# Optimization experiments

Measured on AMD Instinct MI355X. Metric: run time of the kernel, lower is better.

Reference implementation:

```python
import jax, jax.numpy as jnp
import numpy as np

B, S, D, H = 4, 2048, 1024, 16
HD = D // H  # head_dim = 64

def setup_inputs() -> dict:
    key = jax.random.key(0)
    ks = jax.random.split(key, 5)
    scale = 1.0 / np.sqrt(D)
    return {
        "x": jax.random.normal(ks[0], (B, S, D), dtype=jnp.float32),
        "Wqkv": jax.random.normal(ks[1], (D, 3 * D), dtype=jnp.float32) * scale,
        "bqkv": jax.random.normal(ks[2], (3 * D,), dtype=jnp.float32) * 0.01,
        "Wo": jax.random.normal(ks[3], (D, D), dtype=jnp.float32) * scale,
        "bo": jax.random.normal(ks[4], (D,), dtype=jnp.float32) * 0.01,
    }

def reference(x, Wqkv, bqkv, Wo, bo):
    b, s, d = x.shape
    # fused QKV projection: [B,S,3D]
    qkv = jnp.einsum("bsd,de->bse", x, Wqkv) + bqkv
    # [B,S,H,3*HD] -> [B,H,S,3*HD], then chunk into q,k,v per head
    qkv = qkv.reshape(b, s, H, 3 * HD).transpose(0, 2, 1, 3)
    q, k, v = jnp.split(qkv, 3, axis=-1)  # each [B,H,S,HD]
    inv_sqrt_dk = jnp.asarray(1.0 / np.sqrt(HD), dtype=x.dtype)
    scores = jnp.einsum("bhqd,bhkd->bhqk", q, k) * inv_sqrt_dk
    attn = jax.nn.softmax(scores, axis=-1)
    values = jnp.einsum("bhqk,bhkd->bhqd", attn, v)  # [B,H,S,HD]
    # NOTE: source reshapes [B,H,S,HD] -> [B,S,H*HD] WITHOUT permuting back
    # (a quirk of the original code); replicated faithfully.
    values = values.reshape(b, s, d)
    out = jnp.einsum("bsd,de->bse", values, Wo) + bo
    return out
```

## Files before the change

kernel.cpp:

```cpp
#include <hip/hip_runtime.h>
#include <hip/hip_bf16.h>
#include <cstdint>

static constexpr int Bq  = 4;
static constexpr int Sq  = 2048;
static constexpr int Dq  = 1024;
static constexpr int Hq  = 16;
static constexpr int HDq = 64;
static constexpr int ROWS = Bq * Sq;
static constexpr int QKV_N = 3 * Dq;

typedef __bf16 bf16x8 __attribute__((ext_vector_type(8)));
typedef __bf16 bf16x4 __attribute__((ext_vector_type(4)));
typedef __bf16 bf16x2 __attribute__((ext_vector_type(2)));
typedef float  floatx4 __attribute__((ext_vector_type(4)));
typedef float  floatx16 __attribute__((ext_vector_type(16)));
typedef unsigned int uintx4 __attribute__((ext_vector_type(4)));

#define MFMA16(a, b, c) __builtin_amdgcn_mfma_f32_16x16x32_bf16((a), (b), (c), 0, 0, 0)
#define MFMA32(a, b, c) __builtin_amdgcn_mfma_f32_32x32x16_bf16((a), (b), (c), 0, 0, 0)

#define QSCALE 0.18033688011112042f

__device__ __forceinline__ void async16(const void* g, void* l) {
    __builtin_amdgcn_global_load_lds(
        (const __attribute__((address_space(1))) uint32_t*)g,
        (__attribute__((address_space(3))) uint32_t*)l, 16, 0, 0);
}

__global__ __launch_bounds__(256) void prep_kernel(const float4* __restrict__ x4,
                                                   bf16x4* __restrict__ xb4,
                                                   const float* __restrict__ Wqkv,
                                                   __bf16* __restrict__ WqkvT,
                                                   const float* __restrict__ Wo,
                                                   __bf16* __restrict__ WoT) {
    __shared__ float t[32][33];
    const int bx = blockIdx.x;
    if (bx < 8192) {
        int i = bx * 256 + threadIdx.x;
        float4 v = x4[i];
        bf16x4 o;
        o[0] = (__bf16)v.x; o[1] = (__bf16)v.y; o[2] = (__bf16)v.z; o[3] = (__bf16)v.w;
        xb4[i] = o;
        return;
    }
    const float* in; __bf16* out; int K, N, bid;
    if (bx < 8192 + 3072) { bid = bx - 8192;  in = Wqkv; out = WqkvT; K = Dq; N = QKV_N; }
    else                  { bid = bx - 11264; in = Wo;   out = WoT;   K = Dq; N = Dq; }
    const int nt = N / 32;
    const int n0 = (bid % nt) * 32, k0 = (bid / nt) * 32;
    const int c = threadIdx.x & 31, r0 = threadIdx.x >> 5;
#pragma unroll
    for (int rr = 0; rr < 32; rr += 8)
        t[r0 + rr][c] = in[(size_t)(k0 + r0 + rr) * N + n0 + c];
    __syncthreads();
#pragma unroll
    for (int rr = 0; rr < 32; rr += 8)
        out[(size_t)(n0 + r0 + rr) * K + k0 + c] = (__bf16)t[c][r0 + rr];
}

__global__ __launch_bounds__(512, 2) void gemm_qkv_kernel(const __bf16* __restrict__ A,
                                                          const __bf16* __restrict__ BT,
                                                          const float* __restrict__ bias,
                                                          __bf16* __restrict__ qkvb,
                                                          __bf16* __restrict__ Vt) {
    __shared__ __bf16 lds[2][7][64][64];

    const int tid  = threadIdx.x;
    const int lane = tid & 63;
    const int wave = tid >> 6;
    const int wm = wave >> 1;
    const int wn = wave & 1;
    const int l31 = lane & 31;
    const int hi  = lane >> 5;
    const int kx  = l31 & 7;

    const int m0 = blockIdx.y * 256;
    const int n0 = blockIdx.x * 192;

    const int sw = ((lane & 7) ^ (lane >> 3)) * 8;
    const __bf16* gA = A  + (size_t)(m0 + wave * 8 + (lane >> 3)) * 1024 + sw;
    const __bf16* gB = BT + (size_t)(n0 + wave * 8 + (lane >> 3)) * 1024 + sw;

    auto STAGEA = [&](int buf, int u, int ktel) {
        async16(gA + (size_t)u * 65536 + ktel, &lds[buf][u][0][0] + wave * 512 + lane * 8);
    };
    auto STAGEB = [&](int buf, int j, int ktel) {
        async16(gB + (size_t)j * 65536 + ktel, &lds[buf][4 + j][0][0] + wave * 512 + lane * 8);
    };

    floatx16 acc[2][3] = {};

#pragma unroll
    for (int u = 0; u < 4; ++u) STAGEA(0, u, 0);
#pragma unroll
    for (int j = 0; j < 3; ++j) STAGEB(0, j, 0);
#pragma unroll
    for (int u = 0; u < 4; ++u) STAGEA(1, u, 64);
    asm volatile("s_waitcnt vmcnt(4)" ::: "memory");
    __builtin_amdgcn_sched_barrier(0);
    __builtin_amdgcn_s_barrier();

    bf16x8 af[2][4], bf[4];

    for (int t = 0; t < 16; ++t) {
        const int d = t & 1;

#pragma unroll
        for (int fm = 0; fm < 2; ++fm)
#pragma unroll
            for (int ks = 0; ks < 4; ++ks)
                af[fm][ks] = *(const bf16x8*)(&lds[d][wm][fm * 32 + l31][((ks * 2 + hi) ^ kx) * 8]);
        {
            const int br = wn * 96;
#pragma unroll
            for (int ks = 0; ks < 4; ++ks)
                bf[ks] = *(const bf16x8*)(&lds[d][4 + (br >> 6)][(br & 63) + l31][((ks * 2 + hi) ^ kx) * 8]);
        }
        if (t + 1 < 16) {
            STAGEB(d ^ 1, 0, (t + 1) * 64);
            STAGEB(d ^ 1, 1, (t + 1) * 64);
            STAGEB(d ^ 1, 2, (t + 1) * 64);
        }
        __builtin_amdgcn_s_barrier();
        __builtin_amdgcn_s_setprio(1);
#pragma unroll
        for (int ks = 0; ks < 4; ++ks) {
            acc[0][0] = MFMA32(af[0][ks], bf[ks], acc[0][0]);
            acc[1][0] = MFMA32(af[1][ks], bf[ks], acc[1][0]);
        }
        __builtin_amdgcn_s_setprio(0);
        __builtin_amdgcn_s_barrier();

        {
            const int br = wn * 96 + 32;
#pragma unroll
            for (int ks = 0; ks < 4; ++ks)
                bf[ks] = *(const bf16x8*)(&lds[d][4 + (br >> 6)][(br & 63) + l31][((ks * 2 + hi) ^ kx) * 8]);
        }
        if (t + 2 < 16) {
            STAGEA(d, 0, (t + 2) * 64);
            STAGEA(d, 1, (t + 2) * 64);
        }
        __builtin_amdgcn_s_barrier();
        __builtin_amdgcn_s_setprio(1);
#pragma unroll
        for (int ks = 0; ks < 4; ++ks) {
            acc[0][1] = MFMA32(af[0][ks], bf[ks], acc[0][1]);
            acc[1][1] = MFMA32(af[1][ks], bf[ks], acc[1][1]);
        }
        __builtin_amdgcn_s_setprio(0);
        __builtin_amdgcn_s_barrier();

        {
            const int br = wn * 96 + 64;
#pragma unroll
            for (int ks = 0; ks < 4; ++ks)
                bf[ks] = *(const bf16x8*)(&lds[d][4 + (br >> 6)][(br & 63) + l31][((ks * 2 + hi) ^ kx) * 8]);
        }
        if (t + 2 < 16) {
            STAGEA(d, 2, (t + 2) * 64);
            STAGEA(d, 3, (t + 2) * 64);
        }
        __builtin_amdgcn_s_barrier();
        __builtin_amdgcn_s_setprio(1);
#pragma unroll
        for (int ks = 0; ks < 4; ++ks) {
            acc[0][2] = MFMA32(af[0][ks], bf[ks], acc[0][2]);
            acc[1][2] = MFMA32(af[1][ks], bf[ks], acc[1][2]);
        }
        __builtin_amdgcn_s_setprio(0);
        if (t < 14) {
            asm volatile("s_waitcnt vmcnt(4)" ::: "memory");
        } else {
            asm volatile("s_waitcnt vmcnt(0)" ::: "memory");
        }
        __builtin_amdgcn_sched_barrier(0);
        __builtin_amdgcn_s_barrier();
    }

#pragma unroll
    for (int fn = 0; fn < 3; ++fn) {
        const int cm = wn * 96 + fn * 32;
        const int cg = n0 + cm;
        const float bv = bias[cg + l31];
        if (cm >= 128) {
            const int hh = n0 / 192;
            const int dd = cm - 128 + l31;
            const int bb = m0 >> 11;
            const int sb = (m0 & 2047) + wm * 64;
            __bf16* vt = Vt + ((size_t)(bb * Hq + hh) * HDq + dd) * Sq + sb;
#pragma unroll
            for (int fm = 0; fm < 2; ++fm)
#pragma unroll
                for (int g = 0; g < 4; ++g) {
                    bf16x4 vv;
#pragma unroll
                    for (int i = 0; i < 4; ++i) vv[i] = (__bf16)(acc[fm][fn][g * 4 + i] + bv);
                    *(bf16x4*)(vt + fm * 32 + g * 8 + hi * 4) = vv;
                }
        } else {
            const float sc = (cm < 64) ? QSCALE : 1.0f;
#pragma unroll
            for (int fm = 0; fm < 2; ++fm)
#pragma unroll
                for (int r = 0; r < 16; ++r) {
                    int m = m0 + wm * 64 + fm * 32 + (r & 3) + 8 * (r >> 2) + 4 * hi;
                    qkvb[(size_t)m * QKV_N + cg + l31] = (__bf16)((acc[fm][fn][r] + bv) * sc);
                }
        }
    }
}

__global__ __launch_bounds__(256) void gemm_out_kernel(const __bf16* __restrict__ A,
                                                       const __bf16* __restrict__ BT,
                                                       const float* __restrict__ bias,
                                                       float* __restrict__ Cout,
                                                       int M, int N, int K) {
    __shared__ __bf16 As[128 * 32];
    __shared__ __bf16 Bs[128 * 32];

    const int t = threadIdx.x;
    const int lane = t & 63;
    const int wave = t >> 6;
    const int wm = wave & 1, wn = wave >> 1;
    const int l15 = lane & 15;
    const int kg = (lane >> 4) * 8;

    const int m0 = blockIdx.y * 128;
    const int n0 = blockIdx.x * 128;

    const int srow = t >> 2;
    const int scol = (t & 3) * 8;
    const __bf16* ag = A  + (size_t)(m0 + srow) * K + scol;
    const __bf16* bg = BT + (size_t)(n0 + srow) * K + scol;
    __bf16* al = As + t * 8;
    __bf16* bl = Bs + t * 8;

    floatx4 acc[4][4] = {};

    for (int k0 = 0; k0 < K; k0 += 32) {
        __syncthreads();
        async16(ag + k0,                    al);
        async16(ag + (size_t)64 * K + k0,   al + 2048);
        async16(bg + k0,                    bl);
        async16(bg + (size_t)64 * K + k0,   bl + 2048);
        __syncthreads();

        bf16x8 af[4], bfr[4];
#pragma unroll
        for (int mi = 0; mi < 4; ++mi)
            af[mi] = *(const bf16x8*)(As + (wm * 64 + mi * 16 + l15) * 32 + kg);
#pragma unroll
        for (int ni = 0; ni < 4; ++ni)
            bfr[ni] = *(const bf16x8*)(Bs + (wn * 64 + ni * 16 + l15) * 32 + kg);
#pragma unroll
        for (int mi = 0; mi < 4; ++mi)
#pragma unroll
            for (int ni = 0; ni < 4; ++ni)
                acc[mi][ni] = MFMA16(af[mi], bfr[ni], acc[mi][ni]);
    }

    const int r0 = (lane >> 4) * 4;
    const int wn0 = n0 + wn * 64;

#pragma unroll
    for (int ni = 0; ni < 4; ++ni) {
        int col = wn0 + ni * 16 + l15;
        float bv = bias[col];
#pragma unroll
        for (int mi = 0; mi < 4; ++mi) {
#pragma unroll
            for (int i = 0; i < 4; ++i) {
                int row = m0 + wm * 64 + mi * 16 + r0 + i;
                Cout[(size_t)row * N + col] = acc[mi][ni][i] + bv;
            }
        }
    }
}

__global__ __launch_bounds__(256, 2) void attn_kernel(const __bf16* __restrict__ qkv,
                                                      const __bf16* __restrict__ Vt,
                                                      __bf16* __restrict__ v2) {
    const int bh = blockIdx.x;
    const int b = bh >> 4, h = bh & 15;
    const int q0 = blockIdx.y * 256;
    const int tid  = threadIdx.x;
    const int lane = tid & 63;
    const int wave = tid >> 6;
    const int l31  = lane & 31;
    const int hi   = lane >> 5;
    const int kx   = l31 & 7;
    const size_t rs = QKV_N;
    const __bf16* base  = qkv + (size_t)b * Sq * rs + (size_t)h * (3 * HDq);
    const __bf16* vbase = Vt + (size_t)bh * HDq * Sq;

    __shared__ alignas(16) __bf16 Ks[2][64][64];
    __shared__ alignas(16) __bf16 Vs[2][64][64];

    bf16x8 qb[2][4];
#pragma unroll
    for (int qg = 0; qg < 2; ++qg) {
        const __bf16* qr = base + (size_t)(q0 + wave * 64 + qg * 32 + l31) * rs + hi * 8;
#pragma unroll
        for (int st = 0; st < 4; ++st) qb[qg][st] = *(const bf16x8*)(qr + st * 16);
    }

    const int rA = wave * 8 + (lane >> 3);
    const int rB = rA + 32;
    const int sw = ((lane & 7) ^ (rA & 7)) * 8;
    const __bf16* gK0 = base + HDq + (size_t)rA * rs + sw;
    const __bf16* gK1 = base + HDq + (size_t)rB * rs + sw;
    const __bf16* gV0 = vbase + (size_t)rA * Sq + sw;
    const __bf16* gV1 = vbase + (size_t)rB * Sq + sw;
    const int loff0 = wave * 512 + lane * 8;
    const int loff1 = (4 + wave) * 512 + lane * 8;

    auto STAGE = [&](int bufi, int kt) {
        const size_t ko = (size_t)kt * rs;
        async16(gK0 + ko, &Ks[bufi][0][0] + loff0);
        async16(gK1 + ko, &Ks[bufi][0][0] + loff1);
        async16(gV0 + kt, &Vs[bufi][0][0] + loff0);
        async16(gV1 + kt, &Vs[bufi][0][0] + loff1);
    };

    auto softmax_pb = [&](const floatx16& c, float& la, bf16x8* pb) {
        unsigned int W[8];
        float s0 = 0.f, s1 = 0.f;
#pragma unroll
        for (int m = 0; m < 8; ++m) {
            float e0 = __builtin_amdgcn_exp2f(c[2 * m]);
            float e1 = __builtin_amdgcn_exp2f(c[2 * m + 1]);
            s0 += e0; s1 += e1;
            union { bf16x2 v; unsigned int u; } pk;
            pk.v[0] = (__bf16)e0; pk.v[1] = (__bf16)e1;
            W[m] = pk.u;
        }
        la += s0 + s1;
#pragma unroll
        for (int ks = 0; ks < 2; ++ks) {
            auto r0 = __builtin_amdgcn_permlane32_swap(W[ks * 4 + 0], W[ks * 4 + 2], false, false);
            auto r1 = __builtin_amdgcn_permlane32_swap(W[ks * 4 + 1], W[ks * 4 + 3], false, false);
            uintx4 bb; bb[0] = r0[0]; bb[1] = r1[0]; bb[2] = r0[1]; bb[3] = r1[1];
            pb[ks] = __builtin_bit_cast(bf16x8, bb);
        }
    };

    floatx16 o[2][2] = {};
    float la0 = 0.f, la1 = 0.f;

    STAGE(0, 0);
    __syncthreads();

    int cur = 0;
    for (int kt = 0; kt < Sq; kt += 64, cur ^= 1) {
        if (kt + 64 < Sq) STAGE(cur ^ 1, kt + 64);

        bf16x8 ka0[4], ka1[4];
#pragma unroll
        for (int st = 0; st < 4; ++st) {
            ka0[st] = *(const bf16x8*)(&Ks[cur][l31][((st * 2 + hi) ^ kx) * 8]);
            ka1[st] = *(const bf16x8*)(&Ks[cur][32 + l31][((st * 2 + hi) ^ kx) * 8]);
        }
        floatx16 c00 = {}, c01 = {}, c10 = {}, c11 = {};
        __builtin_amdgcn_s_setprio(1);
#pragma unroll
        for (int st = 0; st < 4; ++st) {
            c00 = MFMA32(ka0[st], qb[0][st], c00);
            c10 = MFMA32(ka1[st], qb[0][st], c10);
            c01 = MFMA32(ka0[st], qb[1][st], c01);
            c11 = MFMA32(ka1[st], qb[1][st], c11);
        }
        __builtin_amdgcn_s_setprio(0);

        bf16x8 pb00[2], pb01[2], pb10[2], pb11[2];
        softmax_pb(c00, la0, pb00);
        softmax_pb(c01, la1, pb01);
        __builtin_amdgcn_s_setprio(1);
#pragma unroll
        for (int ks = 0; ks < 2; ++ks) {
            const int kslot = ks * 2 + hi;
            bf16x8 va0 = *(const bf16x8*)(&Vs[cur][l31][(kslot ^ kx) * 8]);
            bf16x8 va1 = *(const bf16x8*)(&Vs[cur][32 + l31][(kslot ^ kx) * 8]);
            o[0][0] = MFMA32(va0, pb00[ks], o[0][0]);
            o[0][1] = MFMA32(va1, pb00[ks], o[0][1]);
            o[1][0] = MFMA32(va0, pb01[ks], o[1][0]);
            o[1][1] = MFMA32(va1, pb01[ks], o[1][1]);
        }
        __builtin_amdgcn_s_setprio(0);
        softmax_pb(c10, la0, pb10);
        softmax_pb(c11, la1, pb11);
        __builtin_amdgcn_s_setprio(1);
#pragma unroll
        for (int ks = 0; ks < 2; ++ks) {
            const int kslot = 4 + ks * 2 + hi;
            bf16x8 va0 = *(const bf16x8*)(&Vs[cur][l31][(kslot ^ kx) * 8]);
            bf16x8 va1 = *(const bf16x8*)(&Vs[cur][32 + l31][(kslot ^ kx) * 8]);
            o[0][0] = MFMA32(va0, pb10[ks], o[0][0]);
            o[0][1] = MFMA32(va1, pb10[ks], o[0][1]);
            o[1][0] = MFMA32(va0, pb11[ks], o[1][0]);
            o[1][1] = MFMA32(va1, pb11[ks], o[1][1]);
        }
        __builtin_amdgcn_s_setprio(0);

        __syncthreads();
    }

#pragma unroll
    for (int qg = 0; qg < 2; ++qg) {
        float lsum = qg ? la1 : la0;
        float l = lsum + __shfl_xor(lsum, 32);
        float rinv = 1.0f / l;
        const int q = q0 + wave * 64 + qg * 32 + l31;
        size_t row = (size_t)b * Sq + h * 128 + (q >> 4);
        __bf16* vrow = v2 + row * Dq + (size_t)(q & 15) * 64;
#pragma unroll
        for (int gg = 0; gg < 4; ++gg) {
            bf16x4 ov;
#pragma unroll
            for (int i = 0; i < 4; ++i) ov[i] = (__bf16)(o[qg][0][gg * 4 + i] * rinv);
            *(bf16x4*)(vrow + gg * 8 + hi * 4) = ov;
#pragma unroll
            for (int i = 0; i < 4; ++i) ov[i] = (__bf16)(o[qg][1][gg * 4 + i] * rinv);
            *(bf16x4*)(vrow + 32 + gg * 8 + hi * 4) = ov;
        }
    }
}

extern "C" void kernel_launch(void* const* d_in, const int* in_sizes, int n_in,
                              void* d_out, int out_size, void* d_ws, size_t ws_size,
                              hipStream_t stream) {
    const float* x    = (const float*)d_in[0];
    const float* Wqkv = (const float*)d_in[1];
    const float* bqkv = (const float*)d_in[2];
    const float* Wo   = (const float*)d_in[3];
    const float* bo   = (const float*)d_in[4];
    float* out = (float*)d_out;

    __bf16* xb    = (__bf16*)d_ws;
    __bf16* WqkvT = xb    + (size_t)ROWS * Dq;
    __bf16* WoT   = WqkvT + (size_t)QKV_N * Dq;
    __bf16* qkvb  = WoT   + (size_t)Dq * Dq;
    __bf16* Vt    = qkvb  + (size_t)ROWS * QKV_N;
    __bf16* v2    = xb;

    prep_kernel<<<12288, 256, 0, stream>>>((const float4*)x, (bf16x4*)xb,
                                           Wqkv, WqkvT, Wo, WoT);

    gemm_qkv_kernel<<<dim3(QKV_N / 192, ROWS / 256), 512, 0, stream>>>(
        xb, WqkvT, bqkv, qkvb, Vt);

    attn_kernel<<<dim3(Bq * Hq, Sq / 256), 256, 0, stream>>>(qkvb, Vt, v2);

    gemm_out_kernel<<<dim3(Dq / 128, ROWS / 128), 256, 0, stream>>>(
        v2, WoT, bo, out, ROWS, Dq, Dq);
}
```

Baseline: 267.5 us.

## Split attention key range across two wave groups and combine partial outputs in LDS

The attention block grows to 512 threads. Two groups of four waves each process half of the key sequence for the same 256 queries, each with its own double-buffered K/V tiles. At the end, one group writes its partial outputs and row sums to shared memory and the other adds them before normalizing and storing. No running max is used, so the partials simply add. This doubles the waves per block to hide latency and halves the serial key loop per wave. In exchange it needs about 70KB of LDS per block, which may limit how many blocks fit per CU, and adds a combine step.

```diff
diff --git a/kernel.cpp b/kernel.cpp
--- a/kernel.cpp
+++ b/kernel.cpp
@@ -279,7 +279,7 @@
     }
 }
 
-__global__ __launch_bounds__(256, 2) void attn_kernel(const __bf16* __restrict__ qkv,
+__global__ __launch_bounds__(512, 2) void attn_kernel(const __bf16* __restrict__ qkv,
                                                       const __bf16* __restrict__ Vt,
                                                       __bf16* __restrict__ v2) {
     const int bh = blockIdx.x;
@@ -288,6 +288,8 @@
     const int tid  = threadIdx.x;
     const int lane = tid & 63;
     const int wave = tid >> 6;
+    const int qs   = wave & 3;
+    const int kgp  = wave >> 2;
     const int l31  = lane & 31;
     const int hi   = lane >> 5;
     const int kx   = l31 & 7;
@@ -295,33 +297,37 @@
     const __bf16* base  = qkv + (size_t)b * Sq * rs + (size_t)h * (3 * HDq);
     const __bf16* vbase = Vt + (size_t)bh * HDq * Sq;
 
-    __shared__ alignas(16) __bf16 Ks[2][64][64];
-    __shared__ alignas(16) __bf16 Vs[2][64][64];
+    __shared__ alignas(16) unsigned char smem[71680];
+    __bf16* KsB = (__bf16*)smem;
+    __bf16* VsB = (__bf16*)(smem + 32768);
 
     bf16x8 qb[2][4];
 #pragma unroll
     for (int qg = 0; qg < 2; ++qg) {
-        const __bf16* qr = base + (size_t)(q0 + wave * 64 + qg * 32 + l31) * rs + hi * 8;
+        const __bf16* qr = base + (size_t)(q0 + qs * 64 + qg * 32 + l31) * rs + hi * 8;
 #pragma unroll
         for (int st = 0; st < 4; ++st) qb[qg][st] = *(const bf16x8*)(qr + st * 16);
     }
 
-    const int rA = wave * 8 + (lane >> 3);
+    const int rA = qs * 8 + (lane >> 3);
     const int rB = rA + 32;
-    const int sw = ((lane & 7) ^ (rA & 7)) * 8;
-    const __bf16* gK0 = base + HDq + (size_t)rA * rs + sw;
-    const __bf16* gK1 = base + HDq + (size_t)rB * rs + sw;
-    const __bf16* gV0 = vbase + (size_t)rA * Sq + sw;
-    const __bf16* gV1 = vbase + (size_t)rB * Sq + sw;
-    const int loff0 = wave * 512 + lane * 8;
-    const int loff1 = (4 + wave) * 512 + lane * 8;
+    const int sw = ((lane & 7) ^ (lane >> 3)) * 8;
+    const int kb = kgp << 10;
+    const __bf16* gK0 = base + HDq + (size_t)(kb + rA) * rs + sw;
+    const __bf16* gK1 = base + HDq + (size_t)(kb + rB) * rs + sw;
+    const __bf16* gV0 = vbase + (size_t)rA * Sq + kb + sw;
+    const __bf16* gV1 = vbase + (size_t)rB * Sq + kb + sw;
+    const int loff0 = qs * 512 + lane * 8;
+    const int loff1 = (4 + qs) * 512 + lane * 8;
 
     auto STAGE = [&](int bufi, int kt) {
         const size_t ko = (size_t)kt * rs;
-        async16(gK0 + ko, &Ks[bufi][0][0] + loff0);
-        async16(gK1 + ko, &Ks[bufi][0][0] + loff1);
-        async16(gV0 + kt, &Vs[bufi][0][0] + loff0);
-        async16(gV1 + kt, &Vs[bufi][0][0] + loff1);
+        __bf16* KsD = KsB + (kgp * 2 + bufi) * 4096;
+        __bf16* VsD = VsB + (kgp * 2 + bufi) * 4096;
+        async16(gK0 + ko, KsD + loff0);
+        async16(gK1 + ko, KsD + loff1);
+        async16(gV0 + kt, VsD + loff0);
+        async16(gV1 + kt, VsD + loff1);
     };
 
     auto softmax_pb = [&](const floatx16& c, float& la, bf16x8* pb) {
@@ -353,14 +359,16 @@
     __syncthreads();
 
     int cur = 0;
-    for (int kt = 0; kt < Sq; kt += 64, cur ^= 1) {
-        if (kt + 64 < Sq) STAGE(cur ^ 1, kt + 64);
+    for (int kt = 0; kt < 1024; kt += 64, cur ^= 1) {
+        if (kt + 64 < 1024) STAGE(cur ^ 1, kt + 64);
+        const __bf16* KsC = KsB + (kgp * 2 + cur) * 4096;
+        const __bf16* VsC = VsB + (kgp * 2 + cur) * 4096;
 
         bf16x8 ka0[4], ka1[4];
 #pragma unroll
         for (int st = 0; st < 4; ++st) {
-            ka0[st] = *(const bf16x8*)(&Ks[cur][l31][((st * 2 + hi) ^ kx) * 8]);
-            ka1[st] = *(const bf16x8*)(&Ks[cur][32 + l31][((st * 2 + hi) ^ kx) * 8]);
+            ka0[st] = *(const bf16x8*)(KsC + l31 * 64 + ((st * 2 + hi) ^ kx) * 8);
+            ka1[st] = *(const bf16x8*)(KsC + (32 + l31) * 64 + ((st * 2 + hi) ^ kx) * 8);
         }
         floatx16 c00 = {}, c01 = {}, c10 = {}, c11 = {};
         __builtin_amdgcn_s_setprio(1);
@@ -380,8 +388,8 @@
 #pragma unroll
         for (int ks = 0; ks < 2; ++ks) {
             const int kslot = ks * 2 + hi;
-            bf16x8 va0 = *(const bf16x8*)(&Vs[cur][l31][(kslot ^ kx) * 8]);
-            bf16x8 va1 = *(const bf16x8*)(&Vs[cur][32 + l31][(kslot ^ kx) * 8]);
+            bf16x8 va0 = *(const bf16x8*)(VsC + l31 * 64 + (kslot ^ kx) * 8);
+            bf16x8 va1 = *(const bf16x8*)(VsC + (32 + l31) * 64 + (kslot ^ kx) * 8);
             o[0][0] = MFMA32(va0, pb00[ks], o[0][0]);
             o[0][1] = MFMA32(va1, pb00[ks], o[0][1]);
             o[1][0] = MFMA32(va0, pb01[ks], o[1][0]);
@@ -394,8 +402,8 @@
 #pragma unroll
         for (int ks = 0; ks < 2; ++ks) {
             const int kslot = 4 + ks * 2 + hi;
-            bf16x8 va0 = *(const bf16x8*)(&Vs[cur][l31][(kslot ^ kx) * 8]);
-            bf16x8 va1 = *(const bf16x8*)(&Vs[cur][32 + l31][(kslot ^ kx) * 8]);
+            bf16x8 va0 = *(const bf16x8*)(VsC + l31 * 64 + (kslot ^ kx) * 8);
+            bf16x8 va1 = *(const bf16x8*)(VsC + (32 + l31) * 64 + (kslot ^ kx) * 8);
             o[0][0] = MFMA32(va0, pb10[ks], o[0][0]);
             o[0][1] = MFMA32(va1, pb10[ks], o[0][1]);
             o[1][0] = MFMA32(va0, pb11[ks], o[1][0]);
@@ -406,23 +414,54 @@
         __syncthreads();
     }
 
-#pragma unroll
-    for (int qg = 0; qg < 2; ++qg) {
-        float lsum = qg ? la1 : la0;
-        float l = lsum + __shfl_xor(lsum, 32);
-        float rinv = 1.0f / l;
-        const int q = q0 + wave * 64 + qg * 32 + l31;
-        size_t row = (size_t)b * Sq + h * 128 + (q >> 4);
-        __bf16* vrow = v2 + row * Dq + (size_t)(q & 15) * 64;
-#pragma unroll
-        for (int gg = 0; gg < 4; ++gg) {
-            bf16x4 ov;
-#pragma unroll
-            for (int i = 0; i < 4; ++i) ov[i] = (__bf16)(o[qg][0][gg * 4 + i] * rinv);
-            *(bf16x4*)(vrow + gg * 8 + hi * 4) = ov;
-#pragma unroll
-            for (int i = 0; i < 4; ++i) ov[i] = (__bf16)(o[qg][1][gg * 4 + i] * rinv);
-            *(bf16x4*)(vrow + 32 + gg * 8 + hi * 4) = ov;
+    float l0 = la0 + __shfl_xor(la0, 32);
+    float l1 = la1 + __shfl_xor(la1, 32);
+
+    float* Ocmb = (float*)smem;
+    float* Lcmb = (float*)(smem + 69632);
+    const int ci = qs * 64 + lane;
+
+    if (kgp) {
+        float* dst = Ocmb + ci * 68;
+#pragma unroll
+        for (int qg = 0; qg < 2; ++qg)
+#pragma unroll
+            for (int dh = 0; dh < 2; ++dh)
+#pragma unroll
+                for (int i = 0; i < 16; ++i)
+                    dst[qg * 32 + dh * 16 + i] = o[qg][dh][i];
+        Lcmb[ci * 2 + 0] = l0;
+        Lcmb[ci * 2 + 1] = l1;
+    }
+    __syncthreads();
+    if (!kgp) {
+        const float* src = Ocmb + ci * 68;
+#pragma unroll
+        for (int qg = 0; qg < 2; ++qg)
+#pragma unroll
+            for (int dh = 0; dh < 2; ++dh)
+#pragma unroll
+                for (int i = 0; i < 16; ++i)
+                    o[qg][dh][i] += src[qg * 32 + dh * 16 + i];
+        l0 += Lcmb[ci * 2 + 0];
+        l1 += Lcmb[ci * 2 + 1];
+
+#pragma unroll
+        for (int qg = 0; qg < 2; ++qg) {
+            float rinv = 1.0f / (qg ? l1 : l0);
+            const int q = q0 + qs * 64 + qg * 32 + l31;
+            size_t row = (size_t)b * Sq + h * 128 + (q >> 4);
+            __bf16* vrow = v2 + row * Dq + (size_t)(q & 15) * 64;
+#pragma unroll
+            for (int gg = 0; gg < 4; ++gg) {
+                bf16x4 ov;
+#pragma unroll
+                for (int i = 0; i < 4; ++i) ov[i] = (__bf16)(o[qg][0][gg * 4 + i] * rinv);
+                *(bf16x4*)(vrow + gg * 8 + hi * 4) = ov;
+#pragma unroll
+                for (int i = 0; i < 4; ++i) ov[i] = (__bf16)(o[qg][1][gg * 4 + i] * rinv);
+                *(bf16x4*)(vrow + 32 + gg * 8 + hi * 4) = ov;
+            }
         }
     }
 }
@@ -450,7 +489,7 @@
     gemm_qkv_kernel<<<dim3(QKV_N / 192, ROWS / 256), 512, 0, stream>>>(
         xb, WqkvT, bqkv, qkvb, Vt);
 
-    attn_kernel<<<dim3(Bq * Hq, Sq / 256), 256, 0, stream>>>(qkvb, Vt, v2);
+    attn_kernel<<<dim3(Bq * Hq, Sq / 256), 512, 0, stream>>>(qkvb, Vt, v2);
 
     gemm_out_kernel<<<dim3(Dq / 128, ROWS / 128), 256, 0, stream>>>(
         v2, WoT, bo, out, ROWS, Dq, Dq);
```

Result: slower. 276.1 us (+3.2%).

## Rewrite output projection GEMM with double-buffered swizzled LDS and 32x32 MFMA

Applied to the files above, without the earlier changes.

The output-projection GEMM moves from a 128x128 tile with one K=32 stage per loop iteration (sync, load, sync, compute) to a 256x128 tile run by 512 threads. It uses K=64 stages, double-buffered LDS with an XOR swizzle to avoid bank conflicts, and 32x32x16 MFMA instructions. Global loads for later stages are issued between the MFMA phases and gated with vmcnt waits, so memory latency overlaps with compute, and setprio raises priority during the MFMA phases. The cost is a larger LDS footprint (96 KB per block) and a hardcoded K dimension, and the manual barrier and vmcnt bookkeeping is fragile.

```diff
diff --git a/kernel.cpp b/kernel.cpp
--- a/kernel.cpp
+++ b/kernel.cpp
@@ -212,70 +212,111 @@
     }
 }
 
-__global__ __launch_bounds__(256) void gemm_out_kernel(const __bf16* __restrict__ A,
-                                                       const __bf16* __restrict__ BT,
-                                                       const float* __restrict__ bias,
-                                                       float* __restrict__ Cout,
-                                                       int M, int N, int K) {
-    __shared__ __bf16 As[128 * 32];
-    __shared__ __bf16 Bs[128 * 32];
-
-    const int t = threadIdx.x;
-    const int lane = t & 63;
-    const int wave = t >> 6;
-    const int wm = wave & 1, wn = wave >> 1;
-    const int l15 = lane & 15;
-    const int kg = (lane >> 4) * 8;
-
-    const int m0 = blockIdx.y * 128;
+__global__ __launch_bounds__(512, 2) void gemm_out_kernel(const __bf16* __restrict__ A,
+                                                          const __bf16* __restrict__ BT,
+                                                          const float* __restrict__ bias,
+                                                          float* __restrict__ Cout) {
+    __shared__ __bf16 lds[2][6][64][64];
+
+    const int tid  = threadIdx.x;
+    const int lane = tid & 63;
+    const int wave = tid >> 6;
+    const int wm = wave >> 1;
+    const int wn = wave & 1;
+    const int l31 = lane & 31;
+    const int hi  = lane >> 5;
+    const int kx  = l31 & 7;
+
+    const int m0 = blockIdx.y * 256;
     const int n0 = blockIdx.x * 128;
 
-    const int srow = t >> 2;
-    const int scol = (t & 3) * 8;
-    const __bf16* ag = A  + (size_t)(m0 + srow) * K + scol;
-    const __bf16* bg = BT + (size_t)(n0 + srow) * K + scol;
-    __bf16* al = As + t * 8;
-    __bf16* bl = Bs + t * 8;
-
-    floatx4 acc[4][4] = {};
-
-    for (int k0 = 0; k0 < K; k0 += 32) {
-        __syncthreads();
-        async16(ag + k0,                    al);
-        async16(ag + (size_t)64 * K + k0,   al + 2048);
-        async16(bg + k0,                    bl);
-        async16(bg + (size_t)64 * K + k0,   bl + 2048);
-        __syncthreads();
-
-        bf16x8 af[4], bfr[4];
-#pragma unroll
-        for (int mi = 0; mi < 4; ++mi)
-            af[mi] = *(const bf16x8*)(As + (wm * 64 + mi * 16 + l15) * 32 + kg);
-#pragma unroll
-        for (int ni = 0; ni < 4; ++ni)
-            bfr[ni] = *(const bf16x8*)(Bs + (wn * 64 + ni * 16 + l15) * 32 + kg);
-#pragma unroll
-        for (int mi = 0; mi < 4; ++mi)
-#pragma unroll
-            for (int ni = 0; ni < 4; ++ni)
-                acc[mi][ni] = MFMA16(af[mi], bfr[ni], acc[mi][ni]);
-    }
-
-    const int r0 = (lane >> 4) * 4;
-    const int wn0 = n0 + wn * 64;
-
-#pragma unroll
-    for (int ni = 0; ni < 4; ++ni) {
-        int col = wn0 + ni * 16 + l15;
-        float bv = bias[col];
-#pragma unroll
-        for (int mi = 0; mi < 4; ++mi) {
-#pragma unroll
-            for (int i = 0; i < 4; ++i) {
-                int row = m0 + wm * 64 + mi * 16 + r0 + i;
-                Cout[(size_t)row * N + col] = acc[mi][ni][i] + bv;
+    const int sw = ((lane & 7) ^ (lane >> 3)) * 8;
+    const __bf16* gA = A  + (size_t)(m0 + wave * 8 + (lane >> 3)) * 1024 + sw;
+    const __bf16* gB = BT + (size_t)(n0 + wave * 8 + (lane >> 3)) * 1024 + sw;
+
+    auto STAGEA = [&](int buf, int u, int ktel) {
+        async16(gA + (size_t)u * 65536 + ktel, &lds[buf][u][0][0] + wave * 512 + lane * 8);
+    };
+    auto STAGEB = [&](int buf, int j, int ktel) {
+        async16(gB + (size_t)j * 65536 + ktel, &lds[buf][4 + j][0][0] + wave * 512 + lane * 8);
+    };
+
+    floatx16 acc[2][2] = {};
+
+#pragma unroll
+    for (int u = 0; u < 4; ++u) STAGEA(0, u, 0);
+#pragma unroll
+    for (int j = 0; j < 2; ++j) STAGEB(0, j, 0);
+#pragma unroll
+    for (int u = 0; u < 4; ++u) STAGEA(1, u, 64);
+    asm volatile("s_waitcnt vmcnt(4)" ::: "memory");
+    __builtin_amdgcn_sched_barrier(0);
+    __builtin_amdgcn_s_barrier();
+
+    bf16x8 af[2][4], bf[4];
+
+    for (int t = 0; t < 16; ++t) {
+        const int d = t & 1;
+
+#pragma unroll
+        for (int fm = 0; fm < 2; ++fm)
+#pragma unroll
+            for (int ks = 0; ks < 4; ++ks)
+                af[fm][ks] = *(const bf16x8*)(&lds[d][wm][fm * 32 + l31][((ks * 2 + hi) ^ kx) * 8]);
+#pragma unroll
+        for (int ks = 0; ks < 4; ++ks)
+            bf[ks] = *(const bf16x8*)(&lds[d][4 + wn][l31][((ks * 2 + hi) ^ kx) * 8]);
+        if (t + 1 < 16) {
+            STAGEB(d ^ 1, 0, (t + 1) * 64);
+            STAGEB(d ^ 1, 1, (t + 1) * 64);
+        }
+        __builtin_amdgcn_s_barrier();
+        __builtin_amdgcn_s_setprio(1);
+#pragma unroll
+        for (int ks = 0; ks < 4; ++ks) {
+            acc[0][0] = MFMA32(af[0][ks], bf[ks], acc[0][0]);
+            acc[1][0] = MFMA32(af[1][ks], bf[ks], acc[1][0]);
+        }
+        __builtin_amdgcn_s_setprio(0);
+        __builtin_amdgcn_s_barrier();
+
+#pragma unroll
+        for (int ks = 0; ks < 4; ++ks)
+            bf[ks] = *(const bf16x8*)(&lds[d][4 + wn][32 + l31][((ks * 2 + hi) ^ kx) * 8]);
+        if (t + 2 < 16) {
+            STAGEA(d, 0, (t + 2) * 64);
+            STAGEA(d, 1, (t + 2) * 64);
+            STAGEA(d, 2, (t + 2) * 64);
+            STAGEA(d, 3, (t + 2) * 64);
+        }
+        __builtin_amdgcn_s_barrier();
+        __builtin_amdgcn_s_setprio(1);
+#pragma unroll
+        for (int ks = 0; ks < 4; ++ks) {
+            acc[0][1] = MFMA32(af[0][ks], bf[ks], acc[0][1]);
+            acc[1][1] = MFMA32(af[1][ks], bf[ks], acc[1][1]);
+        }
+        __builtin_amdgcn_s_setprio(0);
+        if (t < 14) {
+            asm volatile("s_waitcnt vmcnt(4)" ::: "memory");
+        } else {
+            asm volatile("s_waitcnt vmcnt(0)" ::: "memory");
+        }
+        __builtin_amdgcn_sched_barrier(0);
+        __builtin_amdgcn_s_barrier();
+    }
+
+#pragma unroll
+    for (int fn = 0; fn < 2; ++fn) {
+        const int col = n0 + wn * 64 + fn * 32 + l31;
+        const float bv = bias[col];
+#pragma unroll
+        for (int fm = 0; fm < 2; ++fm)
+#pragma unroll
+            for (int r = 0; r < 16; ++r) {
+                int row = m0 + wm * 64 + fm * 32 + (r & 3) + 8 * (r >> 2) + 4 * hi;
+                Cout[(size_t)row * Dq + col] = acc[fm][fn][r] + bv;
             }
-        }
     }
 }
 
@@ -452,6 +493,6 @@
 
     attn_kernel<<<dim3(Bq * Hq, Sq / 256), 256, 0, stream>>>(qkvb, Vt, v2);
 
-    gemm_out_kernel<<<dim3(Dq / 128, ROWS / 128), 256, 0, stream>>>(
-        v2, WoT, bo, out, ROWS, Dq, Dq);
-}
+    gemm_out_kernel<<<dim3(Dq / 128, ROWS / 256), 512, 0, stream>>>(
+        v2, WoT, bo, out);
+}
```

New measurement: 250.8 us. 6.3% less time.
